# Performance work log

Measured on AMD Instinct MI355X. Metric: run time of the kernel, lower is better.

The kernel has to match this reference:

```python
import jax, jax.numpy as jnp
import numpy as np

EPS = 1e-5

def _bn(x, g, b, m, v):
    inv = g / jnp.sqrt(v + EPS)
    return x * inv[None, :, None, None] + (b - m * inv)[None, :, None, None]

def _box_conv(x, y_min, y_max, x_min, x_max):
    # Learnable box filter via integral image + bilinear-interpolated corners.
    # x: (N, C, H, W); box params: (C, B). Output: (N, C*B, H, W), area-normalized.
    N, C, H, W = x.shape
    B = y_min.shape[1]
    # padded integral image (N, C, H+1, W+1)
    I = jnp.pad(jnp.cumsum(jnp.cumsum(x, axis=2), axis=3), ((0, 0), (0, 0), (1, 0), (1, 0)))
    iy = jnp.arange(H, dtype=x.dtype)
    ix = jnp.arange(W, dtype=x.dtype)

    def one_box(Ic, ymn, ymx, xmn, xmx):
        # Ic: (N, H+1, W+1); scalar box extents
        y1 = jnp.clip(iy + ymn, 0.0, H)
        y2 = jnp.clip(iy + ymx + 1.0, 0.0, H)
        x1 = jnp.clip(ix + xmn, 0.0, W)
        x2 = jnp.clip(ix + xmx + 1.0, 0.0, W)

        def interp_y(c):  # (H,) -> (N, H, W+1)
            i0 = jnp.clip(jnp.floor(c), 0.0, H - 1).astype(jnp.int32)
            t = (c - i0)[None, :, None]
            return Ic[:, i0, :] * (1.0 - t) + Ic[:, i0 + 1, :] * t

        Gy1, Gy2 = interp_y(y1), interp_y(y2)

        def interp_x(G, c):  # (N, H, W+1), (W,) -> (N, H, W)
            i0 = jnp.clip(jnp.floor(c), 0.0, W - 1).astype(jnp.int32)
            t = (c - i0)[None, None, :]
            return G[:, :, i0] * (1.0 - t) + G[:, :, i0 + 1] * t

        S = interp_x(Gy2, x2) - interp_x(Gy2, x1) - interp_x(Gy1, x2) + interp_x(Gy1, x1)
        area = (ymx - ymn + 1.0) * (xmx - xmn + 1.0)
        return S / area  # (N, H, W)

    f_b = jax.vmap(one_box, in_axes=(None, 0, 0, 0, 0))   # over boxes
    f_cb = jax.vmap(f_b, in_axes=(1, 0, 0, 0, 0))          # over channels
    out = f_cb(I, y_min, y_max, x_min, x_max)              # (C, B, N, H, W)
    return jnp.transpose(out, (2, 0, 1, 3, 4)).reshape(N, C * B, H, W)


def setup_inputs() -> dict:
    key = jax.random.key(0)
    ks = jax.random.split(key, 20)
    N, Cin, H, W = 32, 256, 56, 56
    Cmid, B = 16, 4
    Cbox = Cmid * B
    Cout = 256
    f32 = jnp.float32
    x = jax.random.normal(ks[0], (N, Cin, H, W), f32)
    w1 = jax.random.normal(ks[1], (Cmid, Cin), f32) * 0.05
    g1 = jax.random.uniform(ks[2], (Cmid,), f32, 0.5, 1.5)
    b1 = jax.random.normal(ks[3], (Cmid,), f32) * 0.1
    m1 = jax.random.normal(ks[4], (Cmid,), f32) * 0.1
    v1 = jax.random.uniform(ks[5], (Cmid,), f32, 0.5, 1.5)
    y_min = -jax.random.uniform(ks[6], (Cmid, B), f32) * 10.0
    y_max = jax.random.uniform(ks[7], (Cmid, B), f32) * 10.0
    x_min = -jax.random.uniform(ks[8], (Cmid, B), f32) * 10.0
    x_max = jax.random.uniform(ks[9], (Cmid, B), f32) * 10.0
    g2 = jax.random.uniform(ks[10], (Cbox,), f32, 0.5, 1.5)
    b2 = jax.random.normal(ks[11], (Cbox,), f32) * 0.1
    m2 = jax.random.normal(ks[12], (Cbox,), f32) * 0.1
    v2 = jax.random.uniform(ks[13], (Cbox,), f32, 0.5, 1.5)
    w3 = jax.random.normal(ks[14], (Cout, Cbox), f32) * 0.05
    g3 = jax.random.uniform(ks[15], (Cout,), f32, 0.5, 1.5)
    b3 = jax.random.normal(ks[16], (Cout,), f32) * 0.1
    m3 = jax.random.normal(ks[17], (Cout,), f32) * 0.1
    v3 = jax.random.uniform(ks[18], (Cout,), f32, 0.5, 1.5)
    return {"x": x, "w1": w1, "g1": g1, "b1": b1, "m1": m1, "v1": v1,
            "y_min": y_min, "y_max": y_max, "x_min": x_min, "x_max": x_max,
            "g2": g2, "b2": b2, "m2": m2, "v2": v2,
            "w3": w3, "g3": g3, "b3": b3, "m3": m3, "v3": v3}


def reference(x, w1, g1, b1, m1, v1, y_min, y_max, x_min, x_max,
              g2, b2, m2, v2, w3, g3, b3, m3, v3):
    out = jnp.einsum('nchw,oc->nohw', x, w1)            # 1x1 conv
    out = jax.nn.relu(_bn(out, g1, b1, m1, v1))
    out = _box_conv(out, y_min, y_max, x_min, x_max)    # (N, Cmid*B, H, W)
    out = jax.nn.relu(_bn(out, g2, b2, m2, v2))
    out = jnp.einsum('nchw,oc->nohw', out, w3)          # 1x1 conv
    out = _bn(out, g3, b3, m3, v3)
    return jax.nn.relu(out + x)
```

## Files before the change

### kernel.cpp

```cpp
#include <hip/hip_runtime.h>
#include <hip/hip_bf16.h>
#include <math.h>

#define EPSB 1e-5f

constexpr int NN = 32, CIN = 256, HH = 56, WW = 56, HW = HH * WW;
constexpr int CMID = 16, NB = 4, CBOX = 64, COUT = 256;

typedef __attribute__((ext_vector_type(8))) short short8;
typedef __attribute__((ext_vector_type(4))) float f32x4;

constexpr size_t WS_W1T   = 0;
constexpr size_t WS_B1F   = WS_W1T + (size_t)CIN * CMID;
constexpr size_t WS_INV3  = WS_B1F + CMID;
constexpr size_t WS_B3F   = WS_INV3 + COUT;
constexpr size_t WS_OUT1  = WS_B3F + COUT;
constexpr size_t WS_W3B   = WS_OUT1 + (size_t)NN * CMID * HW;
constexpr size_t WS_OUT2B = WS_W3B + (size_t)CBOX * COUT / 2;

__global__ __launch_bounds__(256) void k_prep(
    const float* __restrict__ w1, const float* __restrict__ g1,
    const float* __restrict__ b1, const float* __restrict__ m1,
    const float* __restrict__ v1,
    const float* __restrict__ w3, const float* __restrict__ g3,
    const float* __restrict__ b3, const float* __restrict__ m3,
    const float* __restrict__ v3, float* __restrict__ ws) {
  int t = threadIdx.x;
  for (int idx = t; idx < CIN * CMID; idx += 256) {
    int ci = idx >> 4, c = idx & 15;
    float inv = g1[c] / sqrtf(v1[c] + EPSB);
    ws[WS_W1T + idx] = w1[c * CIN + ci] * inv;
  }
  if (t < CMID) {
    float inv = g1[t] / sqrtf(v1[t] + EPSB);
    ws[WS_B1F + t] = b1[t] - m1[t] * inv;
  }
  __hip_bfloat16* w3b = (__hip_bfloat16*)(ws + WS_W3B);
  for (int idx = t; idx < COUT * CBOX; idx += 256) {
    w3b[idx] = __float2bfloat16(w3[idx]);
  }
  {
    float inv = g3[t] / sqrtf(v3[t] + EPSB);
    ws[WS_INV3 + t] = inv;
    ws[WS_B3F + t] = b3[t] - m3[t] * inv;
  }
}

__global__ __launch_bounds__(256) void k1(const float* __restrict__ x,
                                          const float* __restrict__ ws_c,
                                          float* __restrict__ out1) {
  __shared__ float red[4 * 64 * 17];
  int bid = blockIdx.x;
  int n = bid / 49, hwb = (bid % 49) * 64;
  int tid = threadIdx.x;
  int lane = tid & 63;
  int kq = tid >> 6;
  int kq_u = __builtin_amdgcn_readfirstlane(tid) >> 6;

  const float* xb = x + (size_t)n * CIN * HW + hwb + lane;
  const float* w1t = ws_c + WS_W1T;
  float acc[CMID];
#pragma unroll
  for (int c = 0; c < CMID; ++c) acc[c] = 0.f;

  int ci0 = kq_u * 64;
#pragma unroll 8
  for (int i = 0; i < 64; ++i) {
    int ci = ci0 + i;
    float xv = xb[(size_t)ci * HW];
    const float* wr = w1t + ci * CMID;
#pragma unroll
    for (int c = 0; c < CMID; ++c) acc[c] = fmaf(xv, wr[c], acc[c]);
  }
#pragma unroll
  for (int c = 0; c < CMID; ++c) red[kq * 1088 + lane * 17 + c] = acc[c];
  __syncthreads();

  const float* b1f = ws_c + WS_B1F;
#pragma unroll
  for (int j = 0; j < 4; ++j) {
    int o = tid + j * 256;
    int c = o >> 6, pix = o & 63;
    float v = red[pix * 17 + c] + red[1088 + pix * 17 + c] +
              red[2176 + pix * 17 + c] + red[3264 + pix * 17 + c];
    v += b1f[c];
    out1[((size_t)n * CMID + c) * HW + hwb + pix] = fmaxf(v, 0.f);
  }
}

__device__ __forceinline__ float bilin(const float* __restrict__ sI, float y, float x) {
  int iy = min((int)y, 55);
  int ix = min((int)x, 55);
  float ty = y - (float)iy;
  float tx = x - (float)ix;
  const float* r = sI + iy * 57 + ix;
  float a = r[0], b = r[1], cc = r[57], d = r[58];
  float g1v = a * (1.f - ty) + cc * ty;
  float g2v = b * (1.f - ty) + d * ty;
  return g1v * (1.f - tx) + g2v * tx;
}

__global__ __launch_bounds__(512) void k2(
    const float* __restrict__ out1,
    const float* __restrict__ y_min, const float* __restrict__ y_max,
    const float* __restrict__ x_min, const float* __restrict__ x_max,
    const float* __restrict__ g2, const float* __restrict__ b2,
    const float* __restrict__ m2, const float* __restrict__ v2,
    __hip_bfloat16* __restrict__ out2b) {
  __shared__ float sI[57 * 57];
  int bid = blockIdx.x;
  int n = bid >> 4, c = bid & 15;
  int tid = threadIdx.x;

  for (int idx = tid; idx < 57 * 57; idx += 512) sI[idx] = 0.f;
  __syncthreads();
  const float* src = out1 + ((size_t)n * CMID + c) * HW;
  for (int idx = tid; idx < HW; idx += 512) {
    int h = idx / 56, w = idx - h * 56;
    sI[(h + 1) * 57 + (w + 1)] = src[idx];
  }
  __syncthreads();
  if (tid < 56) {
    float run = 0.f;
    int base = (tid + 1) * 57;
    for (int w = 1; w <= 56; ++w) { run += sI[base + w]; sI[base + w] = run; }
  }
  __syncthreads();
  if (tid < 56) {
    float run = 0.f;
    int col = tid + 1;
    for (int h = 1; h <= 56; ++h) { run += sI[h * 57 + col]; sI[h * 57 + col] = run; }
  }
  __syncthreads();

  float pymn[NB], pymx[NB], pxmn[NB], pxmx[NB], pinv[NB], pbi[NB], prar[NB];
#pragma unroll
  for (int b = 0; b < NB; ++b) {
    int cb = c * NB + b;
    pymn[b] = y_min[cb]; pymx[b] = y_max[cb];
    pxmn[b] = x_min[cb]; pxmx[b] = x_max[cb];
    float inv = g2[cb] / sqrtf(v2[cb] + EPSB);
    pinv[b] = inv;
    pbi[b] = b2[cb] - m2[cb] * inv;
    prar[b] = 1.f / ((pymx[b] - pymn[b] + 1.f) * (pxmx[b] - pxmn[b] + 1.f));
  }
  __hip_bfloat16* dst0 = out2b + ((size_t)n * CBOX + c * NB) * HW;

  for (int p = tid; p < HW; p += 512) {
    int h = p / 56, w = p - h * 56;
    float fh = (float)h, fw = (float)w;
#pragma unroll
    for (int b = 0; b < NB; ++b) {
      float y1 = fminf(fmaxf(fh + pymn[b], 0.f), 56.f);
      float y2 = fminf(fmaxf(fh + pymx[b] + 1.f, 0.f), 56.f);
      float x1 = fminf(fmaxf(fw + pxmn[b], 0.f), 56.f);
      float x2 = fminf(fmaxf(fw + pxmx[b] + 1.f, 0.f), 56.f);
      float S = bilin(sI, y2, x2) - bilin(sI, y2, x1) - bilin(sI, y1, x2) + bilin(sI, y1, x1);
      float val = S * prar[b] * pinv[b] + pbi[b];
      dst0[(size_t)b * HW + p] = __float2bfloat16(fmaxf(val, 0.f));
    }
  }
}

__global__ __launch_bounds__(512) void k3(
    const __hip_bfloat16* __restrict__ out2b,
    const __hip_bfloat16* __restrict__ w3b,
    const float* __restrict__ inv3, const float* __restrict__ b3f,
    const float* __restrict__ x, float* __restrict__ out) {
  __shared__ __hip_bfloat16 T[64][72];
  int bid = blockIdx.x;
  int n = bid / 49, hwb = (bid % 49) * 64;
  int tid = threadIdx.x;
  int l = tid & 63, w = tid >> 6;

  {
    const __hip_bfloat16* src = out2b + ((size_t)n * CBOX + l) * HW + hwb + w * 8;
    short8 v = *reinterpret_cast<const short8*>(src);
    const __hip_bfloat16* vp = (const __hip_bfloat16*)&v;
#pragma unroll
    for (int i = 0; i < 8; ++i) T[w * 8 + i][l] = vp[i];
  }

  short8 afrag[2][2];
#pragma unroll
  for (int ot = 0; ot < 2; ++ot)
#pragma unroll
    for (int kh = 0; kh < 2; ++kh) {
      int o = w * 32 + ot * 16 + (l & 15);
      int k0 = kh * 32 + (l >> 4) * 8;
      afrag[ot][kh] = *reinterpret_cast<const short8*>(w3b + o * CBOX + k0);
    }

  __syncthreads();

  short8 bfrag[4][2];
#pragma unroll
  for (int pt = 0; pt < 4; ++pt)
#pragma unroll
    for (int kh = 0; kh < 2; ++kh) {
      int pix = pt * 16 + (l & 15);
      int k0 = kh * 32 + (l >> 4) * 8;
      bfrag[pt][kh] = *reinterpret_cast<const short8*>(&T[pix][k0]);
    }

  f32x4 acc[2][4];
#pragma unroll
  for (int ot = 0; ot < 2; ++ot)
#pragma unroll
    for (int pt = 0; pt < 4; ++pt) acc[ot][pt] = (f32x4)(0.f);

#pragma unroll
  for (int ot = 0; ot < 2; ++ot)
#pragma unroll
    for (int pt = 0; pt < 4; ++pt) {
      acc[ot][pt] = __builtin_amdgcn_mfma_f32_16x16x32_bf16(
          afrag[ot][0], bfrag[pt][0], acc[ot][pt], 0, 0, 0);
      acc[ot][pt] = __builtin_amdgcn_mfma_f32_16x16x32_bf16(
          afrag[ot][1], bfrag[pt][1], acc[ot][pt], 0, 0, 0);
    }

  size_t nbase = (size_t)n * COUT * HW + hwb;
#pragma unroll
  for (int ot = 0; ot < 2; ++ot) {
#pragma unroll
    for (int j = 0; j < 4; ++j) {
      int o = w * 32 + ot * 16 + (l >> 4) * 4 + j;
      float iv = inv3[o], bb = b3f[o];
      size_t rowbase = nbase + (size_t)o * HW;
#pragma unroll
      for (int pt = 0; pt < 4; ++pt) {
        int pix = pt * 16 + (l & 15);
        float v = acc[ot][pt][j] * iv + bb + x[rowbase + pix];
        out[rowbase + pix] = fmaxf(v, 0.f);
      }
    }
  }
}

extern "C" void kernel_launch(void* const* d_in, const int* in_sizes, int n_in,
                              void* d_out, int out_size, void* d_ws, size_t ws_size,
                              hipStream_t stream) {
  const float* x   = (const float*)d_in[0];
  const float* w1  = (const float*)d_in[1];
  const float* g1  = (const float*)d_in[2];
  const float* b1  = (const float*)d_in[3];
  const float* m1  = (const float*)d_in[4];
  const float* v1  = (const float*)d_in[5];
  const float* ymn = (const float*)d_in[6];
  const float* ymx = (const float*)d_in[7];
  const float* xmn = (const float*)d_in[8];
  const float* xmx = (const float*)d_in[9];
  const float* g2  = (const float*)d_in[10];
  const float* b2  = (const float*)d_in[11];
  const float* m2  = (const float*)d_in[12];
  const float* v2  = (const float*)d_in[13];
  const float* w3  = (const float*)d_in[14];
  const float* g3  = (const float*)d_in[15];
  const float* b3  = (const float*)d_in[16];
  const float* m3  = (const float*)d_in[17];
  const float* v3  = (const float*)d_in[18];

  float* ws  = (float*)d_ws;
  float* out = (float*)d_out;
  __hip_bfloat16* w3b   = (__hip_bfloat16*)(ws + WS_W3B);
  __hip_bfloat16* out2b = (__hip_bfloat16*)(ws + WS_OUT2B);

  k_prep<<<1, 256, 0, stream>>>(w1, g1, b1, m1, v1, w3, g3, b3, m3, v3, ws);
  k1<<<NN * 49, 256, 0, stream>>>(x, ws, ws + WS_OUT1);
  k2<<<NN * CMID, 512, 0, stream>>>(ws + WS_OUT1, ymn, ymx, xmn, xmx,
                                    g2, b2, m2, v2, out2b);
  k3<<<NN * 49, 512, 0, stream>>>(out2b, w3b, ws + WS_INV3, ws + WS_B3F, x, out);
}
```

Before: 91.22 us.

## Remove prep kernel by folding weight prep into consumers; parallel scans in box conv

Drops the single-block prep kernel and recomputes the BN-folded conv1 weights in shared memory per block in k1. The bf16 conversion of w3 and the BN3 scale/bias now happen inline in k3. k2 replaces serial per-row/column prefix sums with wavefront shuffle scans, loads its input as float4, and only zeroes the border of the integral image. This removes a serialized tiny launch and long serial scan chains, at the cost of redundant per-block weight/BN recomputation and global loads.

```diff
diff --git a/kernel.cpp b/kernel.cpp
--- a/kernel.cpp
+++ b/kernel.cpp
@@ -10,45 +10,17 @@
 typedef __attribute__((ext_vector_type(8))) short short8;
 typedef __attribute__((ext_vector_type(4))) float f32x4;
 
-constexpr size_t WS_W1T   = 0;
-constexpr size_t WS_B1F   = WS_W1T + (size_t)CIN * CMID;
-constexpr size_t WS_INV3  = WS_B1F + CMID;
-constexpr size_t WS_B3F   = WS_INV3 + COUT;
-constexpr size_t WS_OUT1  = WS_B3F + COUT;
-constexpr size_t WS_W3B   = WS_OUT1 + (size_t)NN * CMID * HW;
-constexpr size_t WS_OUT2B = WS_W3B + (size_t)CBOX * COUT / 2;
-
-__global__ __launch_bounds__(256) void k_prep(
-    const float* __restrict__ w1, const float* __restrict__ g1,
-    const float* __restrict__ b1, const float* __restrict__ m1,
-    const float* __restrict__ v1,
-    const float* __restrict__ w3, const float* __restrict__ g3,
-    const float* __restrict__ b3, const float* __restrict__ m3,
-    const float* __restrict__ v3, float* __restrict__ ws) {
-  int t = threadIdx.x;
-  for (int idx = t; idx < CIN * CMID; idx += 256) {
-    int ci = idx >> 4, c = idx & 15;
-    float inv = g1[c] / sqrtf(v1[c] + EPSB);
-    ws[WS_W1T + idx] = w1[c * CIN + ci] * inv;
-  }
-  if (t < CMID) {
-    float inv = g1[t] / sqrtf(v1[t] + EPSB);
-    ws[WS_B1F + t] = b1[t] - m1[t] * inv;
-  }
-  __hip_bfloat16* w3b = (__hip_bfloat16*)(ws + WS_W3B);
-  for (int idx = t; idx < COUT * CBOX; idx += 256) {
-    w3b[idx] = __float2bfloat16(w3[idx]);
-  }
-  {
-    float inv = g3[t] / sqrtf(v3[t] + EPSB);
-    ws[WS_INV3 + t] = inv;
-    ws[WS_B3F + t] = b3[t] - m3[t] * inv;
-  }
-}
+constexpr size_t WS_OUT1  = 0;
+constexpr size_t WS_OUT2B = WS_OUT1 + (size_t)NN * CMID * HW;
 
 __global__ __launch_bounds__(256) void k1(const float* __restrict__ x,
-                                          const float* __restrict__ ws_c,
+                                          const float* __restrict__ w1,
+                                          const float* __restrict__ g1,
+                                          const float* __restrict__ b1,
+                                          const float* __restrict__ m1,
+                                          const float* __restrict__ v1,
                                           float* __restrict__ out1) {
+  __shared__ float w1s[CIN][CMID];
   __shared__ float red[4 * 64 * 17];
   int bid = blockIdx.x;
   int n = bid / 49, hwb = (bid % 49) * 64;
@@ -57,8 +29,14 @@
   int kq = tid >> 6;
   int kq_u = __builtin_amdgcn_readfirstlane(tid) >> 6;
 
+#pragma unroll
+  for (int c = 0; c < CMID; ++c) {
+    float inv = g1[c] / sqrtf(v1[c] + EPSB);
+    w1s[tid][c] = w1[c * CIN + tid] * inv;
+  }
+  __syncthreads();
+
   const float* xb = x + (size_t)n * CIN * HW + hwb + lane;
-  const float* w1t = ws_c + WS_W1T;
   float acc[CMID];
 #pragma unroll
   for (int c = 0; c < CMID; ++c) acc[c] = 0.f;
@@ -68,22 +46,28 @@
   for (int i = 0; i < 64; ++i) {
     int ci = ci0 + i;
     float xv = xb[(size_t)ci * HW];
-    const float* wr = w1t + ci * CMID;
-#pragma unroll
-    for (int c = 0; c < CMID; ++c) acc[c] = fmaf(xv, wr[c], acc[c]);
+    const f32x4* wv = (const f32x4*)&w1s[ci][0];
+#pragma unroll
+    for (int q = 0; q < 4; ++q) {
+      f32x4 wq = wv[q];
+      acc[q * 4 + 0] = fmaf(xv, wq.x, acc[q * 4 + 0]);
+      acc[q * 4 + 1] = fmaf(xv, wq.y, acc[q * 4 + 1]);
+      acc[q * 4 + 2] = fmaf(xv, wq.z, acc[q * 4 + 2]);
+      acc[q * 4 + 3] = fmaf(xv, wq.w, acc[q * 4 + 3]);
+    }
   }
 #pragma unroll
   for (int c = 0; c < CMID; ++c) red[kq * 1088 + lane * 17 + c] = acc[c];
   __syncthreads();
 
-  const float* b1f = ws_c + WS_B1F;
 #pragma unroll
   for (int j = 0; j < 4; ++j) {
     int o = tid + j * 256;
     int c = o >> 6, pix = o & 63;
     float v = red[pix * 17 + c] + red[1088 + pix * 17 + c] +
               red[2176 + pix * 17 + c] + red[3264 + pix * 17 + c];
-    v += b1f[c];
+    float inv = g1[c] / sqrtf(v1[c] + EPSB);
+    v += b1[c] - m1[c] * inv;
     out1[((size_t)n * CMID + c) * HW + hwb + pix] = fmaxf(v, 0.f);
   }
 }
@@ -111,25 +95,39 @@
   int bid = blockIdx.x;
   int n = bid >> 4, c = bid & 15;
   int tid = threadIdx.x;
-
-  for (int idx = tid; idx < 57 * 57; idx += 512) sI[idx] = 0.f;
-  __syncthreads();
+  int lane = tid & 63, w = tid >> 6;
+
+  if (tid < 57) { sI[tid] = 0.f; sI[tid * 57] = 0.f; }
   const float* src = out1 + ((size_t)n * CMID + c) * HW;
-  for (int idx = tid; idx < HW; idx += 512) {
-    int h = idx / 56, w = idx - h * 56;
-    sI[(h + 1) * 57 + (w + 1)] = src[idx];
-  }
-  __syncthreads();
-  if (tid < 56) {
-    float run = 0.f;
-    int base = (tid + 1) * 57;
-    for (int w = 1; w <= 56; ++w) { run += sI[base + w]; sI[base + w] = run; }
-  }
-  __syncthreads();
-  if (tid < 56) {
-    float run = 0.f;
-    int col = tid + 1;
-    for (int h = 1; h <= 56; ++h) { run += sI[h * 57 + col]; sI[h * 57 + col] = run; }
+  for (int vdx = tid; vdx < HW / 4; vdx += 512) {
+    int p = vdx * 4;
+    int h = p / 56, wq = p - h * 56;
+    f32x4 d = ((const f32x4*)src)[vdx];
+    float* dst = &sI[(h + 1) * 57 + wq + 1];
+    dst[0] = d.x; dst[1] = d.y; dst[2] = d.z; dst[3] = d.w;
+  }
+  __syncthreads();
+
+  for (int r = w; r < 56; r += 8) {
+    float* row = &sI[(r + 1) * 57 + 1];
+    float vv = (lane < 56) ? row[lane] : 0.f;
+#pragma unroll
+    for (int d = 1; d < 64; d <<= 1) {
+      float o = __shfl_up(vv, d, 64);
+      if (lane >= d) vv += o;
+    }
+    if (lane < 56) row[lane] = vv;
+  }
+  __syncthreads();
+  for (int cc = w; cc < 56; cc += 8) {
+    float* col = &sI[57 + cc + 1];
+    float vv = (lane < 56) ? col[lane * 57] : 0.f;
+#pragma unroll
+    for (int d = 1; d < 64; d <<= 1) {
+      float o = __shfl_up(vv, d, 64);
+      if (lane >= d) vv += o;
+    }
+    if (lane < 56) col[lane * 57] = vv;
   }
   __syncthreads();
 
@@ -147,8 +145,8 @@
   __hip_bfloat16* dst0 = out2b + ((size_t)n * CBOX + c * NB) * HW;
 
   for (int p = tid; p < HW; p += 512) {
-    int h = p / 56, w = p - h * 56;
-    float fh = (float)h, fw = (float)w;
+    int h = p / 56, wq = p - h * 56;
+    float fh = (float)h, fw = (float)wq;
 #pragma unroll
     for (int b = 0; b < NB; ++b) {
       float y1 = fminf(fmaxf(fh + pymn[b], 0.f), 56.f);
@@ -164,8 +162,9 @@
 
 __global__ __launch_bounds__(512) void k3(
     const __hip_bfloat16* __restrict__ out2b,
-    const __hip_bfloat16* __restrict__ w3b,
-    const float* __restrict__ inv3, const float* __restrict__ b3f,
+    const float* __restrict__ w3,
+    const float* __restrict__ g3, const float* __restrict__ b3,
+    const float* __restrict__ m3, const float* __restrict__ v3,
     const float* __restrict__ x, float* __restrict__ out) {
   __shared__ __hip_bfloat16 T[64][72];
   int bid = blockIdx.x;
@@ -174,8 +173,8 @@
   int l = tid & 63, w = tid >> 6;
 
   {
-    const __hip_bfloat16* src = out2b + ((size_t)n * CBOX + l) * HW + hwb + w * 8;
-    short8 v = *reinterpret_cast<const short8*>(src);
+    const __hip_bfloat16* srcp = out2b + ((size_t)n * CBOX + l) * HW + hwb + w * 8;
+    short8 v = *reinterpret_cast<const short8*>(srcp);
     const __hip_bfloat16* vp = (const __hip_bfloat16*)&v;
 #pragma unroll
     for (int i = 0; i < 8; ++i) T[w * 8 + i][l] = vp[i];
@@ -188,7 +187,11 @@
     for (int kh = 0; kh < 2; ++kh) {
       int o = w * 32 + ot * 16 + (l & 15);
       int k0 = kh * 32 + (l >> 4) * 8;
-      afrag[ot][kh] = *reinterpret_cast<const short8*>(w3b + o * CBOX + k0);
+      const float* wp = w3 + o * CBOX + k0;
+      union { short8 s; __hip_bfloat16 h[8]; } u;
+#pragma unroll
+      for (int j = 0; j < 8; ++j) u.h[j] = __float2bfloat16(wp[j]);
+      afrag[ot][kh] = u.s;
     }
 
   __syncthreads();
@@ -225,7 +228,8 @@
 #pragma unroll
     for (int j = 0; j < 4; ++j) {
       int o = w * 32 + ot * 16 + (l >> 4) * 4 + j;
-      float iv = inv3[o], bb = b3f[o];
+      float iv = g3[o] / sqrtf(v3[o] + EPSB);
+      float bb = b3[o] - m3[o] * iv;
       size_t rowbase = nbase + (size_t)o * HW;
 #pragma unroll
       for (int pt = 0; pt < 4; ++pt) {
@@ -262,12 +266,10 @@
 
   float* ws  = (float*)d_ws;
   float* out = (float*)d_out;
-  __hip_bfloat16* w3b   = (__hip_bfloat16*)(ws + WS_W3B);
   __hip_bfloat16* out2b = (__hip_bfloat16*)(ws + WS_OUT2B);
 
-  k_prep<<<1, 256, 0, stream>>>(w1, g1, b1, m1, v1, w3, g3, b3, m3, v3, ws);
-  k1<<<NN * 49, 256, 0, stream>>>(x, ws, ws + WS_OUT1);
+  k1<<<NN * 49, 256, 0, stream>>>(x, w1, g1, b1, m1, v1, ws + WS_OUT1);
   k2<<<NN * CMID, 512, 0, stream>>>(ws + WS_OUT1, ymn, ymx, xmn, xmx,
                                     g2, b2, m2, v2, out2b);
-  k3<<<NN * 49, 512, 0, stream>>>(out2b, w3b, ws + WS_INV3, ws + WS_B3F, x, out);
-}
+  k3<<<NN * 49, 512, 0, stream>>>(out2b, w3, g3, b3, m3, v3, x, out);
+}
```

After: 90.11 us. Within noise of the previous version (-1.2%).
